# Kernel optimization log

Measured on AMD Instinct MI355X. Metric: run time of the kernel, lower is better.

The kernel has to match this reference:

```python
import jax, jax.numpy as jnp
import numpy as np

EPS = 1e-5      # BatchNorm1d default eps
K = 4           # branching factor of the ontology tree
HID = 6         # num_hiddens_genotype
LEVEL_SIZES = (64, 16, 4, 1)   # leaves -> root (term_layer_list order)
OFFSETS = (0, 64, 80, 84)      # slices into the stacked [85,...] term params


def setup_inputs() -> dict:
    key = jax.random.key(0)
    ks = jax.random.split(key, 8)
    B, G, GD, NT, NL = 4096, 4096, 24, 85, 64
    f32 = jnp.float32
    return {
        "x": jax.random.normal(ks[0], (B, G), f32),
        "gene_W": jax.random.normal(ks[1], (NL, GD, G), f32) * (1.0 / np.sqrt(G)),
        "gene_b": jnp.zeros((NL, GD), f32),
        "term_W": jax.random.normal(ks[2], (NT, HID, GD), f32) * (1.0 / np.sqrt(GD)),
        "term_b": jnp.zeros((NT, HID), f32),
        "bn_gamma": jnp.ones((NT, HID), f32),
        "bn_beta": jnp.zeros((NT, HID), f32),
        "aux1_W": jax.random.normal(ks[3], (NT, 1, HID), f32) * 0.1,
        "aux1_b": jnp.zeros((NT, 1), f32),
        "aux2_W": jax.random.normal(ks[4], (NT, 1, 1), f32) * 0.1,
        "aux2_b": jnp.zeros((NT, 1), f32),
        "final_W": jax.random.normal(ks[5], (HID, HID), f32) * (1.0 / np.sqrt(HID)),
        "final_b": jnp.zeros((HID,), f32),
        "fbn_gamma": jnp.ones((HID,), f32),
        "fbn_beta": jnp.zeros((HID,), f32),
        "faux_W": jax.random.normal(ks[6], (1, HID), f32) * 0.1,
        "faux_b": jnp.zeros((1,), f32),
        "fout_W": jax.random.normal(ks[7], (1, 1), f32) * 0.1,
        "fout_b": jnp.zeros((1,), f32),
    }


def _bn(z, g, b):
    # training-mode BatchNorm1d: batch mean / biased variance over axis 0
    mu = jnp.mean(z, axis=0, keepdims=True)
    var = jnp.mean((z - mu) ** 2, axis=0, keepdims=True)
    return (z - mu) * jax.lax.rsqrt(var + EPS) * g + b


def _forward(x, gene_W, gene_b, term_W, term_b, bn_gamma, bn_beta,
             aux1_W, aux1_b, aux2_W, aux2_b, final_W, final_b,
             fbn_gamma, fbn_beta, faux_W, faux_b, fout_W, fout_b):
    B = x.shape[0]
    # direct_gene_layers for all 64 leaf terms, batched: [B, 64, 24]
    h_in = jnp.einsum('bg,tkg->btk', x, gene_W) + gene_b
    aux_outs = []
    h = None
    for n, o in zip(LEVEL_SIZES, OFFSETS):  # leaves -> root (DAG topo order)
        if h is not None:
            # concat the K=4 children hidden states of each term: [B,n,K*HID]
            h_in = h.reshape(B, n, K * HID)
        # per-term Linear + tanh + BatchNorm, batched over the n terms
        z = jnp.tanh(jnp.einsum('bti,thi->bth', h_in, term_W[o:o + n]) + term_b[o:o + n])
        h = _bn(z, bn_gamma[o:o + n], bn_beta[o:o + n])  # [B, n, HID]
        # aux head: Linear(HID->1) -> tanh -> Linear(1->1)
        a1 = jnp.tanh(jnp.einsum('bth,toh->bto', h, aux1_W[o:o + n]) + aux1_b[o:o + n])
        a2 = a1 * aux2_W[o:o + n, 0] + aux2_b[o:o + n]   # [B, n, 1]
        aux_outs.append(a2[..., 0])
    root = h[:, 0, :]                                    # [B, HID]
    f = jnp.tanh(root @ final_W.T + final_b)
    mu = jnp.mean(f, axis=0)
    var = jnp.mean((f - mu) ** 2, axis=0)
    f = (f - mu) * jax.lax.rsqrt(var + EPS) * fbn_gamma + fbn_beta
    fa = jnp.tanh(f @ faux_W.T + faux_b)                 # [B, 1]
    pred = jax.nn.sigmoid(fa * fout_W[0, 0] + fout_b)    # [B, 1]
    # aux_out_map flattened in topo order, with 'final' prediction last: [B, 86]
    return jnp.concatenate(aux_outs + [pred], axis=1)


def reference(x, gene_W, gene_b, term_W, term_b, bn_gamma, bn_beta,
              aux1_W, aux1_b, aux2_W, aux2_b, final_W, final_b,
              fbn_gamma, fbn_beta, faux_W, faux_b, fout_W, fout_b):
    return _forward(x, gene_W, gene_b, term_W, term_b, bn_gamma, bn_beta,
                    aux1_W, aux1_b, aux2_W, aux2_b, final_W, final_b,
                    fbn_gamma, fbn_beta, faux_W, faux_b, fout_W, fout_b)
```

## Files before the change

kernel.cpp:

```cpp
#include <hip/hip_runtime.h>
#include <stdint.h>
#include <math.h>

#define EPSV   1e-5f
#define BATCH  4096
#define GDIM   4096
#define NF0    384
#define NSPLIT 8

typedef __attribute__((ext_vector_type(8))) short bf16x8;
typedef __attribute__((ext_vector_type(4))) float f32x4;
typedef __attribute__((ext_vector_type(2))) float f32x2;
typedef __attribute__((ext_vector_type(4))) uint32_t u32x4;

__device__ __forceinline__ uint32_t pkbf(float x, float y) {
    uint32_t a = __float_as_uint(x) + 0x8000u;
    uint32_t b = __float_as_uint(y) + 0x8000u;
    return __builtin_amdgcn_perm(b, a, 0x07060302u);
}
__device__ __forceinline__ uint16_t f2bf(float f) {
    return (uint16_t)((__float_as_uint(f) + 0x8000u) >> 16);
}
__device__ __forceinline__ float blo(uint32_t v) {
    union { uint32_t u; float f; } x; x.u = v << 16; return x.f;
}
__device__ __forceinline__ float bhi(uint32_t v) {
    union { uint32_t u; float f; } x; x.u = v & 0xffff0000u; return x.f;
}
__device__ __forceinline__ void glds16(const uint16_t* g, short* l) {
    __builtin_amdgcn_global_load_lds(
        (const __attribute__((address_space(1))) void*)g,
        (__attribute__((address_space(3))) void*)l, 16, 0, 0);
}

__global__ __launch_bounds__(256) void prep_kernel(
    const float* __restrict__ gene_W,
    const float* __restrict__ term_W, const float* __restrict__ term_b,
    const float* __restrict__ gene_b,
    uint16_t* __restrict__ m0, float* __restrict__ stats)
{
    const int tid = threadIdx.x;
    if (blockIdx.x == 0) {
        for (int j = tid; j < 1040; j += 256) stats[j] = 0.f;
        for (int f = tid; f < NF0; f += 256) {
            const int t = f / 6, h = f - t * 6;
            float b = term_b[f];
#pragma unroll
            for (int i = 0; i < 24; ++i)
                b += term_W[t * 144 + h * 24 + i] * gene_b[t * 24 + i];
            stats[1040 + f] = b;
        }
    }
    __shared__ float Wl[144];
    const int bid = blockIdx.x;
    const int t = bid >> 4;
    const int g = ((bid & 15) << 8) + tid;
    if (tid < 144) Wl[tid] = term_W[t * 144 + tid];
    __syncthreads();
    float gw[24];
#pragma unroll
    for (int i = 0; i < 24; ++i)
        gw[i] = gene_W[((size_t)t * 24 + i) * GDIM + g];
#pragma unroll
    for (int h = 0; h < 6; ++h) {
        float s = 0.f;
#pragma unroll
        for (int i = 0; i < 24; ++i) s += Wl[h * 24 + i] * gw[i];
        m0[((size_t)(t * 6 + h)) * GDIM + g] = f2bf(s);
    }
}

__global__ __launch_bounds__(256) void gemm_glds(
    const float* __restrict__ A32, const uint16_t* __restrict__ Bw,
    uint16_t* __restrict__ P, int KC)
{
    const int N = NF0, K = GDIM;
    __shared__ short sA[128 * 32];
    __shared__ short sB[128 * 32];
    const int tid  = threadIdx.x;
    const int m0   = blockIdx.y * 128, n0 = blockIdx.x * 128;
    const int kbase = blockIdx.z * KC;
    uint16_t* Cp = P + (size_t)blockIdx.z * ((size_t)BATCH * NF0);
    const int wave = tid >> 6, lane = tid & 63;
    const int wm   = (wave & 1) << 6, wn = (wave >> 1) << 6;
    const int lm   = lane & 15, quad = lane >> 4;

    f32x4 acc[4][4];
#pragma unroll
    for (int i = 0; i < 4; ++i)
#pragma unroll
        for (int j = 0; j < 4; ++j) acc[i][j] = (f32x4){0.f, 0.f, 0.f, 0.f};

    const int r0  = tid >> 2;
    const int c0e = (tid & 3) << 3;
    const float*    gA = A32 + (size_t)(m0 + r0) * K + kbase + c0e;
    const uint16_t* gB = Bw  + (size_t)(n0 + r0) * K + kbase + c0e;
    short* la0 = &sA[tid * 8];
    short* la1 = &sA[2048 + tid * 8];
    short* lb0 = &sB[tid * 8];
    short* lb1 = &sB[2048 + tid * 8];
    const size_t rowskip = (size_t)64 * K;

    for (int k0 = 0; k0 < KC; k0 += 32) {
        __syncthreads();
        glds16(gB + k0,           lb0);
        glds16(gB + rowskip + k0, lb1);
        f32x4 a0 = *(const f32x4*)(gA + k0);
        f32x4 a1 = *(const f32x4*)(gA + k0 + 4);
        f32x4 a2 = *(const f32x4*)(gA + rowskip + k0);
        f32x4 a3 = *(const f32x4*)(gA + rowskip + k0 + 4);
        u32x4 pa0 = (u32x4){pkbf(a0[0],a0[1]), pkbf(a0[2],a0[3]),
                            pkbf(a1[0],a1[1]), pkbf(a1[2],a1[3])};
        u32x4 pa1 = (u32x4){pkbf(a2[0],a2[1]), pkbf(a2[2],a2[3]),
                            pkbf(a3[0],a3[1]), pkbf(a3[2],a3[3])};
        *(u32x4*)la0 = pa0;
        *(u32x4*)la1 = pa1;
        __syncthreads();
        bf16x8 af[4], bfr[4];
#pragma unroll
        for (int m = 0; m < 4; ++m)
            af[m]  = *(const bf16x8*)&sA[(wm + m * 16 + lm) * 32 + quad * 8];
#pragma unroll
        for (int n = 0; n < 4; ++n)
            bfr[n] = *(const bf16x8*)&sB[(wn + n * 16 + lm) * 32 + quad * 8];
#pragma unroll
        for (int m = 0; m < 4; ++m)
#pragma unroll
            for (int n = 0; n < 4; ++n)
                acc[m][n] = __builtin_amdgcn_mfma_f32_16x16x32_bf16(
                    af[m], bfr[n], acc[m][n], 0, 0, 0);
    }
#pragma unroll
    for (int n = 0; n < 4; ++n) {
        const int col = n0 + wn + n * 16 + lm;
#pragma unroll
        for (int m = 0; m < 4; ++m) {
            const int row = m0 + wm + m * 16 + (quad << 2);
            uint16_t* cp = Cp + (size_t)row * N + col;
#pragma unroll
            for (int r = 0; r < 4; ++r) cp[(size_t)r * N] = f2bf(acc[m][n][r]);
        }
    }
}

__global__ __launch_bounds__(256) void lzero_kernel(
    const uint16_t* __restrict__ P, const float* __restrict__ bias0,
    float* __restrict__ z0, float* __restrict__ st0)
{
    __shared__ float red[4 * 768];
    const int tid  = threadIdx.x;
    const int lane = tid & 63, wave = tid >> 6;
    const uint32_t* P32 = (const uint32_t*)P;

    const f32x2 b0 = ((const f32x2*)bias0)[lane];
    const f32x2 b1 = ((const f32x2*)(bias0 + 128))[lane];
    const f32x2 b2 = ((const f32x2*)(bias0 + 256))[lane];

    float s[6], q[6];
#pragma unroll
    for (int k = 0; k < 6; ++k) { s[k] = 0.f; q[k] = 0.f; }

    const int rbase = blockIdx.x * 8 + wave * 2;
    for (int rl = 0; rl < 2; ++rl) {
        const int r = rbase + rl;
        float a0 = b0[0], a1 = b0[1], a2 = b1[0], a3 = b1[1], a4 = b2[0], a5 = b2[1];
        const uint32_t* pr = P32 + (size_t)r * 192 + lane;
#pragma unroll
        for (int z = 0; z < NSPLIT; ++z) {
            const uint32_t* p = pr + (size_t)z * ((size_t)BATCH * 192);
            uint32_t u0 = p[0], u1 = p[64], u2 = p[128];
            a0 += blo(u0); a1 += bhi(u0);
            a2 += blo(u1); a3 += bhi(u1);
            a4 += blo(u2); a5 += bhi(u2);
        }
        float z0v = tanhf(a0), z1v = tanhf(a1), z2v = tanhf(a2);
        float z3v = tanhf(a3), z4v = tanhf(a4), z5v = tanhf(a5);
        f32x2* zr = (f32x2*)(z0 + (size_t)r * NF0);
        zr[lane]       = (f32x2){z0v, z1v};
        zr[64 + lane]  = (f32x2){z2v, z3v};
        zr[128 + lane] = (f32x2){z4v, z5v};
        s[0] += z0v; q[0] += z0v * z0v;
        s[1] += z1v; q[1] += z1v * z1v;
        s[2] += z2v; q[2] += z2v * z2v;
        s[3] += z3v; q[3] += z3v * z3v;
        s[4] += z4v; q[4] += z4v * z4v;
        s[5] += z5v; q[5] += z5v * z5v;
    }
    float* rw = &red[wave * 768 + lane * 12];
#pragma unroll
    for (int k = 0; k < 6; ++k) { rw[k] = s[k]; rw[6 + k] = q[k]; }
    __syncthreads();
    for (int idx = tid; idx < 768; idx += 256) {
        float v = red[idx] + red[768 + idx] + red[1536 + idx] + red[2304 + idx];
        const int l = idx / 12, k = idx - l * 12;
        const int k6 = k % 6;
        const int f = (k6 >> 1) * 128 + 2 * l + (k6 & 1);
        atomicAdd(&st0[(k >= 6 ? NF0 : 0) + f], v);
    }
}

template <int N, int ROWS, int OFF, int PREV_OFF>
__global__ __launch_bounds__(256) void level_kernel(
    const float* __restrict__ in, float* __restrict__ z_out,
    const float* __restrict__ stats_prev, float* __restrict__ stats_out,
    const float* __restrict__ term_W, const float* __restrict__ term_b,
    const float* __restrict__ bn_gamma, const float* __restrict__ bn_beta,
    const float* __restrict__ aux1_W, const float* __restrict__ aux1_b,
    const float* __restrict__ aux2_W, const float* __restrict__ aux2_b,
    float* __restrict__ out)
{
    constexpr int IN_W  = 24 * N;
    constexpr int NFv   = 6 * N;
    constexpr int NG    = 256 / N;
    constexpr int ITERS = (ROWS * N) / 256;
    constexpr int NPREV = 4 * N;

    __shared__ float Wl[144 * N];
    __shared__ float tbl[6 * N];
    __shared__ float aA[IN_W];
    __shared__ float aC[IN_W];
    __shared__ float a1wL[6 * NPREV];
    __shared__ float a1bL[NPREV], a2wL[NPREV], a2bL[NPREV];
    __shared__ float ps[NG * NFv], pq[NG * NFv];

    const int tid = threadIdx.x;
    for (int idx = tid; idx < 144 * N; idx += 256) {
        int t = idx / 144, fh = idx - t * 144;
        Wl[fh * N + t] = term_W[(OFF + t) * 144 + fh];
    }
    for (int idx = tid; idx < 6 * N; idx += 256) {
        int t = idx / 6, h = idx - t * 6;
        tbl[h * N + t] = term_b[(OFF + t) * 6 + h];
    }
    {
        const float invB = 1.0f / BATCH;
        for (int j = tid; j < IN_W; j += 256) {
            float s = stats_prev[j], q = stats_prev[IN_W + j];
            float mu = s * invB;
            float var = q * invB - mu * mu;
            float rstd = rsqrtf(var + EPSV);
            float a = rstd * bn_gamma[PREV_OFF * 6 + j];
            int t = j / 24, i = j - t * 24;
            aA[i * N + t] = a;
            aC[i * N + t] = bn_beta[PREV_OFF * 6 + j] - mu * a;
        }
        for (int idx = tid; idx < 6 * NPREV; idx += 256) {
            int t = idx / 6, h = idx - t * 6;
            a1wL[h * NPREV + t] = aux1_W[(PREV_OFF + t) * 6 + h];
        }
        for (int t = tid; t < NPREV; t += 256) {
            a1bL[t] = aux1_b[PREV_OFF + t];
            a2wL[t] = aux2_W[PREV_OFF + t];
            a2bL[t] = aux2_b[PREV_OFF + t];
        }
    }
    __syncthreads();

    const int term = tid & (N - 1);
    const int grp  = tid / N;
    float s6[6], q6[6];
#pragma unroll
    for (int h = 0; h < 6; ++h) { s6[h] = 0.f; q6[h] = 0.f; }

    for (int it = 0; it < ITERS; ++it) {
        const int r = blockIdx.x * ROWS + it * NG + grp;
        const float* inrow = in + (size_t)r * IN_W + term * 24;
        float hv[24];
#pragma unroll
        for (int i4 = 0; i4 < 6; ++i4) {
            f32x4 v = *(const f32x4*)(inrow + 4 * i4);
            hv[4*i4+0] = v[0]; hv[4*i4+1] = v[1];
            hv[4*i4+2] = v[2]; hv[4*i4+3] = v[3];
        }
#pragma unroll
        for (int i = 0; i < 24; ++i)
            hv[i] = hv[i] * aA[i * N + term] + aC[i * N + term];
#pragma unroll
        for (int s = 0; s < 4; ++s) {
            const int tp = term * 4 + s;
            float acc = a1bL[tp];
#pragma unroll
            for (int h2 = 0; h2 < 6; ++h2) acc += hv[s * 6 + h2] * a1wL[h2 * NPREV + tp];
            float a1 = tanhf(acc);
            out[(size_t)r * 86 + PREV_OFF + tp] = a1 * a2wL[tp] + a2bL[tp];
        }
        float za[6];
#pragma unroll
        for (int h = 0; h < 6; ++h) za[h] = tbl[h * N + term];
#pragma unroll
        for (int i = 0; i < 24; ++i) {
            const float x = hv[i];
#pragma unroll
            for (int h = 0; h < 6; ++h) za[h] += x * Wl[(h * 24 + i) * N + term];
        }
        float* zr = z_out + (size_t)r * NFv + term * 6;
#pragma unroll
        for (int h = 0; h < 6; ++h) {
            float z = tanhf(za[h]);
            zr[h] = z;
            s6[h] += z;
            q6[h] += z * z;
        }
    }
#pragma unroll
    for (int h = 0; h < 6; ++h) {
        ps[grp * NFv + term * 6 + h] = s6[h];
        pq[grp * NFv + term * 6 + h] = q6[h];
    }
    __syncthreads();
    for (int f = tid; f < NFv; f += 256) {
        float s = 0.f, q = 0.f;
        for (int g2 = 0; g2 < NG; ++g2) { s += ps[g2 * NFv + f]; q += pq[g2 * NFv + f]; }
        atomicAdd(&stats_out[f], s);
        atomicAdd(&stats_out[NFv + f], q);
    }
}

__global__ __launch_bounds__(1024) void final_fused(
    const float* __restrict__ z3, const float* __restrict__ st3,
    const float* __restrict__ bn_gamma, const float* __restrict__ bn_beta,
    const float* __restrict__ aux1_W, const float* __restrict__ aux1_b,
    const float* __restrict__ aux2_W, const float* __restrict__ aux2_b,
    const float* __restrict__ final_W, const float* __restrict__ final_b,
    const float* __restrict__ fbn_gamma, const float* __restrict__ fbn_beta,
    const float* __restrict__ faux_W, const float* __restrict__ faux_b,
    const float* __restrict__ fout_W, const float* __restrict__ fout_b,
    float* __restrict__ out)
{
    __shared__ float wred[16][12];
    __shared__ float fstat[12];
    const int tid = threadIdx.x;
    const float invB = 1.0f / BATCH;
    float a[6], c[6], fw[36], fbv[6];
#pragma unroll
    for (int j = 0; j < 6; ++j) {
        float s = st3[j], q = st3[6 + j];
        float mu = s * invB, var = q * invB - mu * mu;
        float rstd = rsqrtf(var + EPSV);
        a[j] = rstd * bn_gamma[84 * 6 + j];
        c[j] = bn_beta[84 * 6 + j] - mu * a[j];
        fbv[j] = final_b[j];
    }
#pragma unroll
    for (int j = 0; j < 36; ++j) fw[j] = final_W[j];

    float s6[6], q6[6];
#pragma unroll
    for (int j = 0; j < 6; ++j) { s6[j] = 0.f; q6[j] = 0.f; }

    for (int i = 0; i < 4; ++i) {
        const int r = i * 1024 + tid;
        float h[6];
#pragma unroll
        for (int j = 0; j < 6; ++j) h[j] = z3[(size_t)r * 6 + j] * a[j] + c[j];
        float acc = aux1_b[84];
#pragma unroll
        for (int j = 0; j < 6; ++j) acc += h[j] * aux1_W[84 * 6 + j];
        out[(size_t)r * 86 + 84] = tanhf(acc) * aux2_W[84] + aux2_b[84];
#pragma unroll
        for (int j = 0; j < 6; ++j) {
            float s = fbv[j];
#pragma unroll
            for (int k = 0; k < 6; ++k) s += h[k] * fw[j * 6 + k];
            float f = tanhf(s);
            s6[j] += f; q6[j] += f * f;
        }
    }
#pragma unroll
    for (int off = 32; off >= 1; off >>= 1) {
#pragma unroll
        for (int j = 0; j < 6; ++j) {
            s6[j] += __shfl_xor(s6[j], off, 64);
            q6[j] += __shfl_xor(q6[j], off, 64);
        }
    }
    const int wv = tid >> 6, ln = tid & 63;
    if (ln == 0) {
#pragma unroll
        for (int j = 0; j < 6; ++j) { wred[wv][j] = s6[j]; wred[wv][6 + j] = q6[j]; }
    }
    __syncthreads();
    if (tid < 12) {
        float s = 0.f;
#pragma unroll
        for (int w = 0; w < 16; ++w) s += wred[w][tid];
        fstat[tid] = s;
    }
    __syncthreads();
    float av[6], cv[6];
#pragma unroll
    for (int j = 0; j < 6; ++j) {
        float mu = fstat[j] * invB, var = fstat[6 + j] * invB - mu * mu;
        float rstd = rsqrtf(var + EPSV);
        av[j] = rstd * fbn_gamma[j];
        cv[j] = fbn_beta[j] - mu * av[j];
    }
    const float fxb0 = faux_b[0], foW0 = fout_W[0], fob0 = fout_b[0];
    for (int i = 0; i < 4; ++i) {
        const int r = i * 1024 + tid;
        float h[6];
#pragma unroll
        for (int j = 0; j < 6; ++j) h[j] = z3[(size_t)r * 6 + j] * a[j] + c[j];
        float acc2 = fxb0;
#pragma unroll
        for (int j = 0; j < 6; ++j) {
            float s = fbv[j];
#pragma unroll
            for (int k = 0; k < 6; ++k) s += h[k] * fw[j * 6 + k];
            float fn = tanhf(s) * av[j] + cv[j];
            acc2 += fn * faux_W[j];
        }
        float fa  = tanhf(acc2);
        float pre = fa * foW0 + fob0;
        out[(size_t)r * 86 + 85] = 1.0f / (1.0f + expf(-pre));
    }
}

extern "C" void kernel_launch(void* const* d_in, const int* in_sizes, int n_in,
                              void* d_out, int out_size, void* d_ws, size_t ws_size,
                              hipStream_t stream)
{
    const float* x      = (const float*)d_in[0];
    const float* gene_W = (const float*)d_in[1];
    const float* gene_b = (const float*)d_in[2];
    const float* term_W = (const float*)d_in[3];
    const float* term_b = (const float*)d_in[4];
    const float* bn_g   = (const float*)d_in[5];
    const float* bn_b   = (const float*)d_in[6];
    const float* a1W    = (const float*)d_in[7];
    const float* a1b    = (const float*)d_in[8];
    const float* a2W    = (const float*)d_in[9];
    const float* a2b    = (const float*)d_in[10];
    const float* fW     = (const float*)d_in[11];
    const float* fb     = (const float*)d_in[12];
    const float* fbn_g  = (const float*)d_in[13];
    const float* fbn_b  = (const float*)d_in[14];
    const float* fxW    = (const float*)d_in[15];
    const float* fxb    = (const float*)d_in[16];
    const float* foW    = (const float*)d_in[17];
    const float* fob    = (const float*)d_in[18];
    float* out = (float*)d_out;

    const size_t M0B = (size_t)NF0 * GDIM * 2;
    const size_t PB  = (size_t)NSPLIT * BATCH * NF0 * 2;
    const size_t Z0B = (size_t)BATCH * NF0 * 4;

    char* ws = (char*)d_ws;
    uint16_t* m0b  = (uint16_t*)ws;
    uint16_t* pbuf = (uint16_t*)(ws + M0B);
    float*    z0   = (float*)(ws + M0B + PB);
    float*    z1   = (float*)(ws + M0B + PB + Z0B);
    float*    z2   = (float*)(ws + M0B + PB + Z0B + 1572864);
    float*    z3   = (float*)(ws + M0B + PB + Z0B + 1572864 + 393216);
    float*    stats = (float*)(ws + M0B + PB + Z0B + 1572864 + 393216 + 98304);
    float* st0 = stats;
    float* st1 = stats + 768;
    float* st2 = stats + 960;
    float* st3 = stats + 1008;
    float* bias0 = stats + 1040;

    prep_kernel<<<1024, 256, 0, stream>>>(gene_W, term_W, term_b, gene_b,
                                          m0b, stats);
    gemm_glds<<<dim3(3, 32, NSPLIT), 256, 0, stream>>>(x, m0b, pbuf, GDIM / NSPLIT);
    lzero_kernel<<<512, 256, 0, stream>>>(pbuf, bias0, z0, st0);
    level_kernel<16, 16, 64, 0><<<256, 256, 0, stream>>>(
        z0, z1, st0, st1, term_W, term_b, bn_g, bn_b, a1W, a1b, a2W, a2b, out);
    level_kernel<4, 64, 80, 64><<<64, 256, 0, stream>>>(
        z1, z2, st1, st2, term_W, term_b, bn_g, bn_b, a1W, a1b, a2W, a2b, out);
    level_kernel<1, 256, 84, 80><<<16, 256, 0, stream>>>(
        z2, z3, st2, st3, term_W, term_b, bn_g, bn_b, a1W, a1b, a2W, a2b, out);
    final_fused<<<1, 1024, 0, stream>>>(
        z3, st3, bn_g, bn_b, a1W, a1b, a2W, a2b, fW, fb,
        fbn_g, fbn_b, fxW, fxb, foW, fob, out);
}
```

Measured before the change: 252.5 us.

## Double-buffer B tile and prefetch next A/B k-slice in gemm_glds

Measured after the change: 257.3 us. Within noise of the previous version (+1.9%).

```diff
diff --git a/kernel.cpp b/kernel.cpp
--- a/kernel.cpp
+++ b/kernel.cpp
@@ -76,7 +76,7 @@
 {
     const int N = NF0, K = GDIM;
     __shared__ short sA[128 * 32];
-    __shared__ short sB[128 * 32];
+    __shared__ short sB[2][128 * 32];
     const int tid  = threadIdx.x;
     const int m0   = blockIdx.y * 128, n0 = blockIdx.x * 128;
     const int kbase = blockIdx.z * KC;
@@ -97,32 +97,69 @@
     const uint16_t* gB = Bw  + (size_t)(n0 + r0) * K + kbase + c0e;
     short* la0 = &sA[tid * 8];
     short* la1 = &sA[2048 + tid * 8];
-    short* lb0 = &sB[tid * 8];
-    short* lb1 = &sB[2048 + tid * 8];
     const size_t rowskip = (size_t)64 * K;
 
-    for (int k0 = 0; k0 < KC; k0 += 32) {
-        __syncthreads();
-        glds16(gB + k0,           lb0);
-        glds16(gB + rowskip + k0, lb1);
-        f32x4 a0 = *(const f32x4*)(gA + k0);
-        f32x4 a1 = *(const f32x4*)(gA + k0 + 4);
-        f32x4 a2 = *(const f32x4*)(gA + rowskip + k0);
-        f32x4 a3 = *(const f32x4*)(gA + rowskip + k0 + 4);
+    glds16(gB,            &sB[0][tid * 8]);
+    glds16(gB + rowskip,  &sB[0][2048 + tid * 8]);
+    f32x4 a0 = *(const f32x4*)(gA);
+    f32x4 a1 = *(const f32x4*)(gA + 4);
+    f32x4 a2 = *(const f32x4*)(gA + rowskip);
+    f32x4 a3 = *(const f32x4*)(gA + rowskip + 4);
+
+    int cur = 0;
+    for (int k0 = 0; k0 < KC - 32; k0 += 32) {
+        const int kn = k0 + 32;
+        glds16(gB + kn,           &sB[cur ^ 1][tid * 8]);
+        glds16(gB + rowskip + kn, &sB[cur ^ 1][2048 + tid * 8]);
+        f32x4 n0v = *(const f32x4*)(gA + kn);
+        f32x4 n1v = *(const f32x4*)(gA + kn + 4);
+        f32x4 n2v = *(const f32x4*)(gA + rowskip + kn);
+        f32x4 n3v = *(const f32x4*)(gA + rowskip + kn + 4);
+        asm volatile("s_waitcnt vmcnt(6)" ::: "memory");
         u32x4 pa0 = (u32x4){pkbf(a0[0],a0[1]), pkbf(a0[2],a0[3]),
                             pkbf(a1[0],a1[1]), pkbf(a1[2],a1[3])};
         u32x4 pa1 = (u32x4){pkbf(a2[0],a2[1]), pkbf(a2[2],a2[3]),
                             pkbf(a3[0],a3[1]), pkbf(a3[2],a3[3])};
         *(u32x4*)la0 = pa0;
         *(u32x4*)la1 = pa1;
-        __syncthreads();
+        asm volatile("s_waitcnt lgkmcnt(0)" ::: "memory");
+        __builtin_amdgcn_s_barrier();
         bf16x8 af[4], bfr[4];
 #pragma unroll
         for (int m = 0; m < 4; ++m)
             af[m]  = *(const bf16x8*)&sA[(wm + m * 16 + lm) * 32 + quad * 8];
 #pragma unroll
         for (int n = 0; n < 4; ++n)
-            bfr[n] = *(const bf16x8*)&sB[(wn + n * 16 + lm) * 32 + quad * 8];
+            bfr[n] = *(const bf16x8*)&sB[cur][(wn + n * 16 + lm) * 32 + quad * 8];
+#pragma unroll
+        for (int m = 0; m < 4; ++m)
+#pragma unroll
+            for (int n = 0; n < 4; ++n)
+                acc[m][n] = __builtin_amdgcn_mfma_f32_16x16x32_bf16(
+                    af[m], bfr[n], acc[m][n], 0, 0, 0);
+        __builtin_amdgcn_s_barrier();
+        a0 = n0v; a1 = n1v; a2 = n2v; a3 = n3v;
+        cur ^= 1;
+    }
+    asm volatile("s_waitcnt vmcnt(0)" ::: "memory");
+    {
+        u32x4 pa0 = (u32x4){pkbf(a0[0],a0[1]), pkbf(a0[2],a0[3]),
+                            pkbf(a1[0],a1[1]), pkbf(a1[2],a1[3])};
+        u32x4 pa1 = (u32x4){pkbf(a2[0],a2[1]), pkbf(a2[2],a2[3]),
+                            pkbf(a3[0],a3[1]), pkbf(a3[2],a3[3])};
+        *(u32x4*)la0 = pa0;
+        *(u32x4*)la1 = pa1;
+    }
+    asm volatile("s_waitcnt lgkmcnt(0)" ::: "memory");
+    __builtin_amdgcn_s_barrier();
+    {
+        bf16x8 af[4], bfr[4];
+#pragma unroll
+        for (int m = 0; m < 4; ++m)
+            af[m]  = *(const bf16x8*)&sA[(wm + m * 16 + lm) * 32 + quad * 8];
+#pragma unroll
+        for (int n = 0; n < 4; ++n)
+            bfr[n] = *(const bf16x8*)&sB[cur][(wn + n * 16 + lm) * 32 + quad * 8];
 #pragma unroll
         for (int m = 0; m < 4; ++m)
 #pragma unroll
```
